# Kernel optimization log

Measured on AMD Instinct MI355X. Metric: run time of the kernel, lower is better.

The kernel has to match this reference:

```python
import jax, jax.numpy as jnp
import numpy as np


def _lstm(x, k, r, b, return_sequences=True):
    # Keras LSTM: gate order i, f, c(g), o; sigmoid recurrent activation, tanh activation.
    # x: [B,T,D], k: [D,4H], r: [H,4H], b: [4H]
    B = x.shape[0]
    H = r.shape[0]
    xk = jnp.einsum('btd,dh->bth', x, k) + b  # precompute input projections for all steps

    def step(carry, xk_t):
        h, c = carry
        z = xk_t + h @ r
        i, f, g, o = jnp.split(z, 4, axis=-1)
        i = jax.nn.sigmoid(i)
        f = jax.nn.sigmoid(f)
        g = jnp.tanh(g)
        o = jax.nn.sigmoid(o)
        c = f * c + i * g
        h = o * jnp.tanh(c)
        return (h, c), h

    h0 = jnp.zeros((B, H), x.dtype)
    (hT, _), hs = jax.lax.scan(step, (h0, jnp.zeros_like(h0)), jnp.swapaxes(xk, 0, 1))
    if return_sequences:
        return jnp.swapaxes(hs, 0, 1)  # [B,T,H]
    return hT  # [B,H]


def _bias(h):
    # Keras unit_forget_bias=True: forget-gate bias initialized to 1
    return jnp.zeros((4 * h,), jnp.float32).at[h:2 * h].set(1.0)


def setup_inputs() -> dict:
    key = jax.random.key(0)
    ks = jax.random.split(key, 20)
    B, T, D = 128, 512, 64
    s = 0.05

    def n(k, shape):
        return jax.random.normal(k, shape, jnp.float32) * s

    inp = {"x": jax.random.normal(ks[0], (B, T, D), jnp.float32)}
    lstm_dims = [(D, 640), (640, 400), (400, 256), (256, 256)]
    i = 1
    for li, (din, h) in enumerate(lstm_dims, 1):
        inp[f"k{li}"] = n(ks[i], (din, 4 * h))
        inp[f"r{li}"] = n(ks[i + 1], (h, 4 * h))
        inp[f"b{li}"] = _bias(h)
        i += 2
    dense_dims = [(256, 512), (512, 256), (256, 128), (128, 64), (64, 16), (16, 3)]
    for li, (din, dout) in enumerate(dense_dims, 1):
        inp[f"wd{li}"] = n(ks[i], (din, dout))
        inp[f"bd{li}"] = jnp.zeros((dout,), jnp.float32)
        i += 1
    return inp


def reference(x, k1, r1, b1, k2, r2, b2, k3, r3, b3, k4, r4, b4,
              wd1, bd1, wd2, bd2, wd3, bd3, wd4, bd4, wd5, bd5, wd6, bd6):
    h = _lstm(x, k1, r1, b1, return_sequences=True)
    h = _lstm(h, k2, r2, b2, return_sequences=True)
    h = _lstm(h, k3, r3, b3, return_sequences=True)
    h = _lstm(h, k4, r4, b4, return_sequences=False)  # [B, 256]
    # Dropout layers are identity at inference (Keras call without training=True)
    h = jax.nn.relu(h @ wd1 + bd1)
    h = jax.nn.relu(h @ wd2 + bd2)
    h = jax.nn.relu(h @ wd3 + bd3)
    h = jax.nn.relu(h @ wd4 + bd4)
    h = jax.nn.relu(h @ wd5 + bd5)
    logits = h @ wd6 + bd6
    return jax.nn.softmax(logits, axis=-1)  # class_count=3 branch
```

## Files before the change

kernel.cpp:

```cpp
#include <hip/hip_runtime.h>
#include <hip/hip_cooperative_groups.h>
#include <cstdint>
#include <cstddef>

namespace cg = cooperative_groups;

typedef _Float16 f16;
typedef _Float16 h8v  __attribute__((ext_vector_type(8)));
typedef float    f32x4 __attribute__((ext_vector_type(4)));

static constexpr int BATCH  = 128;
static constexpr int TSTEPS = 512;
static constexpr int NT     = 256;

static constexpr int TB1 = 80, TB2 = 100, TB3 = 32, TB4 = 32;
static constexpr int TNB   = TB1 + TB2 + TB3 + TB4;
static constexpr int NGRID = TNB + 4;

template<int RING> struct WS {
  static constexpr size_t XT  = 0;
  static constexpr size_t H1  = XT + 512ull * 128 * 64 * 2;
  static constexpr size_t H2  = H1 + (size_t)RING * 128 * 640 * 2 + 64;
  static constexpr size_t H3  = H2 + (size_t)RING * 128 * 400 * 2 + 64;
  static constexpr size_t H4  = H3 + (size_t)RING * 128 * 256 * 2 + 64;
  static constexpr size_t PK1 = H4 + (size_t)RING * 128 * 256 * 2 + 64;
  static constexpr size_t PK2 = PK1 + (size_t)TB1 * 32 * 704  * 2;
  static constexpr size_t PK3 = PK2 + (size_t)TB2 * 16 * 1056 * 2;
  static constexpr size_t PK4 = PK3 + (size_t)TB3 * 32 * 672  * 2;
  static constexpr size_t BAR = PK4 + (size_t)TB4 * 32 * 512  * 2;
  static constexpr size_t ZERO= BAR + 8192;
  static constexpr size_t END = ZERO + 163840;
};

struct KParams {
  const float *x;
  const float *k1, *r1, *b1, *k2, *r2, *b2, *k3, *r3, *b3, *k4, *r4, *b4;
  const float *wd1, *bd1, *wd2, *bd2, *wd3, *bd3, *wd4, *bd4, *wd5, *bd5, *wd6, *bd6;
  float *out;
  char *ws;
};

__device__ __forceinline__ float sigm(float v) { return 1.f / (1.f + expf(-v)); }

__device__ __forceinline__ uint64_t c_load8(const void* p) {
  return __hip_atomic_load((const uint64_t*)p, __ATOMIC_RELAXED, __HIP_MEMORY_SCOPE_AGENT);
}
__device__ __forceinline__ void c_store8(void* p, uint64_t v) {
  __hip_atomic_store((uint64_t*)p, v, __ATOMIC_RELAXED, __HIP_MEMORY_SCOPE_AGENT);
}
__device__ __forceinline__ unsigned short c_load2(const void* p) {
  return __hip_atomic_load((const unsigned short*)p, __ATOMIC_RELAXED, __HIP_MEMORY_SCOPE_AGENT);
}
__device__ __forceinline__ unsigned u_load(const unsigned* p) {
  return __hip_atomic_load(p, __ATOMIC_RELAXED, __HIP_MEMORY_SCOPE_AGENT);
}
__device__ __forceinline__ void u_store(unsigned* p, unsigned v) {
  __hip_atomic_store(p, v, __ATOMIC_RELAXED, __HIP_MEMORY_SCOPE_AGENT);
}
__device__ __forceinline__ void acq_fence() {
  __builtin_amdgcn_fence(__ATOMIC_ACQUIRE, "agent");
}

template<int NBLK>
__device__ void control_role(unsigned* U, int first, int lidx) {
  const int w = threadIdx.x >> 6, lane = threadIdx.x & 63;
  int cand = 1;
  while (cand <= TSTEPS) {
    unsigned v0 = (lane < NBLK)      ? u_load(&U[4 * (first + lane) + w])      : 0xFFFFFFFFu;
    unsigned v1 = (lane + 64 < NBLK) ? u_load(&U[4 * (first + lane + 64) + w]) : 0xFFFFFFFFu;
    unsigned v = v0 < v1 ? v0 : v1;
    if (__all((int)(v >= (unsigned)cand))) {
      if (lane < 16) u_store(&U[1024 + lane * 64 + lidx * 4 + w], (unsigned)cand);
      ++cand;
    }
  }
}

__device__ void prepack_layer(const float* __restrict__ gk, const float* __restrict__ gr,
                              f16* __restrict__ pack, int DIN, int H, int NJ, int KPAD,
                              int TB, int gtid, int gstr) {
  const int KREAL = DIN + H;
  const int NGC = 4 * NJ;
  const long total = (long)TB * NGC * KPAD;
  for (long e = gtid; e < total; e += gstr) {
    const int  k   = (int)(e % KPAD);
    const long r   = e / KPAD;
    const int  n   = (int)(r % NGC);
    const int  blk = (int)(r / NGC);
    const int  g   = n / NJ, jj = n % NJ;
    const int  j   = blk * NJ + jj;
    float v = 0.f;
    if (k < DIN)        v = gk[(size_t)k * 4 * H + (size_t)g * H + j];
    else if (k < KREAL) v = gr[(size_t)(k - DIN) * 4 * H + (size_t)g * H + j];
    pack[e] = (f16)v;
  }
}

#define FETCH(PP, CC) do { \
  _Pragma("unroll") \
  for (int ii_ = 0; ii_ < C; ++ii_) { \
    const int ks_ = (CC) * C + ii_; \
    if (ks_ < KS) { \
      const int k_ = ks_ * 32 + kg; \
      _Pragma("unroll") \
      for (int m_ = 0; m_ < 2; ++m_) { \
        const int bmv_ = m_ ? bm1 : bm0; \
        uint4 v_ = make_uint4(0u, 0u, 0u, 0u); \
        if constexpr (SEQM) { \
          if (k_ < DIN)        v_ = *(const uint4*)(inP + (size_t)bmv_ * DIN + k_); \
          else if (k_ < KREAL) v_ = *(const uint4*)(inH + (size_t)bmv_ * H + (k_ - DIN)); \
        } else { \
          if (k_ < DIN) { \
            const f16* p_ = inP + (size_t)bmv_ * DIN + k_; \
            if constexpr (SEQIN) { \
              ((uint64_t*)&v_)[0] = *(const uint64_t*)p_; \
              ((uint64_t*)&v_)[1] = *(const uint64_t*)(p_ + 4); \
            } else { \
              ((uint64_t*)&v_)[0] = c_load8(p_); \
              ((uint64_t*)&v_)[1] = c_load8(p_ + 4); \
            } \
          } else if (k_ < KREAL) { \
            const f16* p_ = inH + (size_t)bmv_ * H + (k_ - DIN); \
            ((uint64_t*)&v_)[0] = c_load8(p_); \
            ((uint64_t*)&v_)[1] = c_load8(p_ + 4); \
          } \
        } \
        ab[PP][ii_][m_] = v_; \
      } \
    } \
  } \
} while (0)

#define COMPUTE(PP, CC) do { \
  _Pragma("unroll") \
  for (int ii_ = 0; ii_ < C; ++ii_) { \
    const int ks_ = (CC) * C + ii_; \
    if (ks_ < KS) { \
      const int kb_ = ks_ * 32; \
      h8v bf_[NTI]; \
      _Pragma("unroll") \
      for (int nt_ = 0; nt_ < NTI; ++nt_) \
        bf_[nt_] = *(const h8v*)(wlds + (size_t)(nt_ * 16 + l15) * WROW + kb_ + kg); \
      _Pragma("unroll") \
      for (int m_ = 0; m_ < 2; ++m_) { \
        union { uint4 u; h8v v; } af_; \
        af_.u = ab[PP][ii_][m_]; \
        _Pragma("unroll") \
        for (int nt_ = 0; nt_ < NTI; ++nt_) \
          acc[m_][nt_] = __builtin_amdgcn_mfma_f32_16x16x32_f16(af_.v, bf_[nt_], acc[m_][nt_], 0, 0, 0); \
      } \
    } \
  } \
} while (0)

#define WAITOWN do { \
  bool c_ = (lane != 0) || (rcO >= t); \
  while (!__all((int)c_)) { \
    if (!c_) { rcO = (int)u_load(&relp[LIDX * 4 + w]); c_ = (rcO >= t); } \
  } \
} while (0)

template<int DIN, int H, int NJ, int LIDX, bool SEQIN, int RING>
__device__ void lstm_role(int blk, int bid, const f16* lo_base, f16* ownH,
                          const f16* pack, const float* __restrict__ gbias,
                          const f16* zreg, char* smem, unsigned* U) {
  constexpr bool SEQM = (RING == TSTEPS);
  constexpr int KREAL = DIN + H;
  constexpr int KS    = (KREAL + 31) / 32;
  constexpr int KPAD  = KS * 32;
  constexpr int NGC   = 4 * NJ;
  constexpr int NTI   = NGC / 16;
  constexpr int WROW  = KPAD + 8;
  constexpr int ZROW  = 132;
  constexpr int C     = 6;
  constexpr int NC    = (KS + C - 1) / C;
  constexpr int KSX   = DIN / 32;
  constexpr int CH    = KSX / C;
  static_assert(NC <= 6, "NC");
  static_assert(CH <= NC - 1, "CH");
  static_assert(NGC % 16 == 0 && (DIN % 8) == 0 && (KREAL % 8) == 0, "geom");

  const int tid  = threadIdx.x;
  const int w    = tid >> 6, lane = tid & 63;
  const int l15  = lane & 15;
  const int kg   = (lane >> 4) * 8;
  const int bm0  = w * 32 + l15;
  const int bm1  = bm0 + 16;

  f16*   wlds = (f16*)smem;
  float* z    = (float*)(smem + (size_t)NGC * WROW * 2);

  {
    const f16* src = pack + (size_t)blk * NGC * KPAD;
    constexpr int RU = KPAD / 8;
    for (int u = tid; u < NGC * RU; u += NT) {
      const int n = u / RU, k8 = u % RU;
      *(uint4*)(wlds + (size_t)n * WROW + k8 * 8) =
          *(const uint4*)(src + (size_t)n * KPAD + k8 * 8);
    }
  }
  __syncthreads();

  constexpr int JW = NJ / 4;
  const int be  = 32 * w + lane / JW;
  const int jg  = lane % JW;
  const bool epi = (lane < 32 * JW);
  const int j0  = blk * NJ + jg * 4;
  f32x4 bias4[4] = {};
  if (epi) {
    #pragma unroll
    for (int g = 0; g < 4; ++g) bias4[g] = *(const f32x4*)(gbias + (size_t)g * H + j0);
  }
  float cst[4] = {0.f, 0.f, 0.f, 0.f};

  const unsigned* relp = &U[1024 + (bid & 15) * 64];
  int rcI = 0, rcO = 0, rcD = 0;
  (void)rcI; (void)rcD;

  for (int t = 0; t < TSTEPS; ++t) {
    {
      bool c = true;
      if constexpr (LIDX > 0) { if (lane == 0) c = (rcI >= t + 1); }
      if constexpr (CH == 0)  { if (lane == 1) c = (rcO >= t); }
      if constexpr (!SEQM && LIDX < 3) { if (lane == 2) c = (rcD >= t - (RING - 1)); }
      while (!__all((int)c)) {
        if (!c) {
          if constexpr (LIDX > 0) {
            if (lane == 0) { rcI = (int)u_load(&relp[(LIDX - 1) * 4 + w]); c = (rcI >= t + 1); }
          }
          if constexpr (CH == 0) {
            if (lane == 1) { rcO = (int)u_load(&relp[LIDX * 4 + w]); c = (rcO >= t); }
          }
          if constexpr (!SEQM && LIDX < 3) {
            if (lane == 2) { rcD = (int)u_load(&relp[(LIDX + 1) * 4 + w]); c = (rcD >= t - (RING - 1)); }
          }
        }
      }
    }

    const f16* inP = SEQIN ? lo_base + (size_t)t * DIN * BATCH
                           : lo_base + (size_t)(t & (RING - 1)) * DIN * BATCH;
    const f16* inH = (t == 0) ? zreg
                              : ownH + (size_t)((t - 1) & (RING - 1)) * H * BATCH;

    f32x4 acc[2][NTI];
    {
      const f32x4 zz = {0.f, 0.f, 0.f, 0.f};
      #pragma unroll
      for (int m_ = 0; m_ < 2; ++m_)
        #pragma unroll
        for (int nt_ = 0; nt_ < NTI; ++nt_) acc[m_][nt_] = zz;
    }

    uint4 ab[3][C][2];

    FETCH(0, 0);
    if constexpr (NC > 1) { if constexpr (CH == 1) WAITOWN; FETCH(1, 1); }
    if constexpr (NC > 2) { if constexpr (CH == 2) WAITOWN; FETCH(2, 2); }
    COMPUTE(0, 0);
    if constexpr (NC > 1) { if constexpr (NC > 3) { if constexpr (CH == 3) WAITOWN; FETCH(0, 3); } COMPUTE(1, 1); }
    if constexpr (NC > 2) { if constexpr (NC > 4) { if constexpr (CH == 4) WAITOWN; FETCH(1, 4); } COMPUTE(2, 2); }
    if constexpr (NC > 3) { if constexpr (NC > 5) { if constexpr (CH == 5) WAITOWN; FETCH(2, 5); } COMPUTE(0, 3); }
    if constexpr (NC > 4) COMPUTE(1, 4);
    if constexpr (NC > 5) COMPUTE(2, 5);

    #pragma unroll
    for (int m_ = 0; m_ < 2; ++m_)
      #pragma unroll
      for (int nt_ = 0; nt_ < NTI; ++nt_)
        *(f32x4*)(z + (size_t)(nt_ * 16 + l15) * ZROW + w * 32 + m_ * 16 + (lane >> 4) * 4) =
            acc[m_][nt_];

    if (epi) {
      float vi[4], vf[4], vg[4], vo[4];
      #pragma unroll
      for (int q = 0; q < 4; ++q) {
        const int nn = jg * 4 + q;
        vi[q] = z[(size_t)(0 * NJ + nn) * ZROW + be];
        vf[q] = z[(size_t)(1 * NJ + nn) * ZROW + be];
        vg[q] = z[(size_t)(2 * NJ + nn) * ZROW + be];
        vo[q] = z[(size_t)(3 * NJ + nn) * ZROW + be];
      }
      union { f16 h[4]; uint64_t u; } o;
      #pragma unroll
      for (int q = 0; q < 4; ++q) {
        const float ig = sigm(vi[q] + bias4[0][q]);
        const float fg = sigm(vf[q] + bias4[1][q]);
        const float gg = tanhf(vg[q] + bias4[2][q]);
        const float og = sigm(vo[q] + bias4[3][q]);
        cst[q] = fg * cst[q] + ig * gg;
        o.h[q] = (f16)(og * tanhf(cst[q]));
      }
      c_store8(ownH + (size_t)(t & (RING - 1)) * H * BATCH + (size_t)be * H + j0, o.u);
    }
    asm volatile("s_waitcnt vmcnt(0)" ::: "memory");
    if (lane == 0) u_store(&U[4 * bid + w], (unsigned)(t + 1));
  }
}
#undef FETCH
#undef COMPUTE
#undef WAITOWN

__device__ void dense_stage(const float* in, float* outb,
                            const float* __restrict__ w, const float* __restrict__ bias,
                            int din, int dout, bool relu) {
  for (int jc = threadIdx.x; jc < dout; jc += NT) {
    float s = bias[jc];
    for (int d = 0; d < din; ++d) s += in[d] * w[(size_t)d * dout + jc];
    outb[jc] = relu ? fmaxf(s, 0.f) : s;
  }
  __syncthreads();
}

constexpr size_t cmax(size_t a, size_t b) { return a > b ? a : b; }
constexpr size_t wlz(int NGC, int KPAD) {
  return (size_t)NGC * (KPAD + 8) * 2 + (size_t)NGC * 132 * 4;
}
static constexpr size_t SMEM_BYTES =
    cmax(cmax(wlz(32, 704), wlz(16, 1056)),
         cmax(cmax(wlz(32, 672), wlz(32, 512)), (size_t)4096));
static_assert(SMEM_BYTES <= 65536, "LDS");

template<int RING>
__global__ __launch_bounds__(NT, 1) void fused_kernel(KParams p) {
  using L = WS<RING>;
  cg::grid_group grid = cg::this_grid();
  __shared__ __attribute__((aligned(16))) char smem[SMEM_BYTES];

  char* ws = p.ws;
  unsigned* U = (unsigned*)(ws + L::BAR);
  const f16* zreg = (const f16*)(ws + L::ZERO);
  const int tid  = threadIdx.x;
  const int bid  = blockIdx.x;
  const int gtid = bid * NT + tid;
  const int gstr = NGRID * NT;

  prepack_layer(p.k1, p.r1, (f16*)(ws + L::PK1), 64,  640, 8, 704,  TB1, gtid, gstr);
  prepack_layer(p.k2, p.r2, (f16*)(ws + L::PK2), 640, 400, 4, 1056, TB2, gtid, gstr);
  prepack_layer(p.k3, p.r3, (f16*)(ws + L::PK3), 400, 256, 8, 672,  TB3, gtid, gstr);
  prepack_layer(p.k4, p.r4, (f16*)(ws + L::PK4), 256, 256, 8, 512,  TB4, gtid, gstr);

  {
    f16* xT = (f16*)(ws + L::XT);
    const long total = (long)TSTEPS * BATCH * 8;
    for (long u = gtid; u < total; u += gstr) {
      const int  d8 = (int)(u & 7);
      const long r  = u >> 3;
      const int  b  = (int)(r & (BATCH - 1));
      const int  t  = (int)(r >> 7);
      const float* src = p.x + ((size_t)b * TSTEPS + t) * 64 + d8 * 8;
      const float4 v0 = *(const float4*)src;
      const float4 v1 = *(const float4*)(src + 4);
      h8v o;
      o[0] = (f16)v0.x; o[1] = (f16)v0.y; o[2] = (f16)v0.z; o[3] = (f16)v0.w;
      o[4] = (f16)v1.x; o[5] = (f16)v1.y; o[6] = (f16)v1.z; o[7] = (f16)v1.w;
      *(h8v*)(xT + ((size_t)t * BATCH + b) * 64 + d8 * 8) = o;
    }
  }

  grid.sync();
  acq_fence();

  constexpr int TRB2 = TB1, TRB3 = TB1 + TB2, TRB4 = TB1 + TB2 + TB3;
  if (bid >= TNB) {
    const int l = bid - TNB;
    if (l == 0)      control_role<TB1>(U, 0,    0);
    else if (l == 1) control_role<TB2>(U, TRB2, 1);
    else if (l == 2) control_role<TB3>(U, TRB3, 2);
    else             control_role<TB4>(U, TRB4, 3);
  } else if (bid < TRB2) {
    lstm_role< 64, 640, 8, 0, true , RING>(bid, bid, (const f16*)(ws + L::XT),
        (f16*)(ws + L::H1), (const f16*)(ws + L::PK1), p.b1, zreg, smem, U);
  } else if (bid < TRB3) {
    lstm_role<640, 400, 4, 1, false, RING>(bid - TRB2, bid, (const f16*)(ws + L::H1),
        (f16*)(ws + L::H2), (const f16*)(ws + L::PK2), p.b2, zreg, smem, U);
  } else if (bid < TRB4) {
    lstm_role<400, 256, 8, 2, false, RING>(bid - TRB3, bid, (const f16*)(ws + L::H2),
        (f16*)(ws + L::H3), (const f16*)(ws + L::PK3), p.b3, zreg, smem, U);
  } else {
    lstm_role<256, 256, 8, 3, false, RING>(bid - TRB4, bid, (const f16*)(ws + L::H3),
        (f16*)(ws + L::H4), (const f16*)(ws + L::PK4), p.b4, zreg, smem, U);
  }

  if (bid < BATCH) {
    if (tid < 64) {
      bool c = (tid >= 4);
      int rc = 0;
      while (!__all((int)c)) {
        if (!c) {
          rc = (int)u_load(&U[1024 + (bid & 15) * 64 + 3 * 4 + tid]);
          c = (rc >= TSTEPS);
        }
      }
    }
    __syncthreads();
    const int b = bid;
    float* A = (float*)smem;
    float* B = (float*)smem + 512;
    const f16* h4 = (const f16*)(ws + L::H4)
                  + (size_t)((TSTEPS - 1) & (RING - 1)) * 256 * BATCH + (size_t)b * 256;
    for (int d = tid; d < 256; d += NT) {
      union { unsigned short u; f16 h; } cc;
      cc.u = c_load2(h4 + d);
      A[d] = (float)cc.h;
    }
    __syncthreads();
    dense_stage(A, B, p.wd1, p.bd1, 256, 512, true);
    dense_stage(B, A, p.wd2, p.bd2, 512, 256, true);
    dense_stage(A, B, p.wd3, p.bd3, 256, 128, true);
    dense_stage(B, A, p.wd4, p.bd4, 128, 64,  true);
    dense_stage(A, B, p.wd5, p.bd5, 64,  16,  true);
    dense_stage(B, A, p.wd6, p.bd6, 16,  3,   false);
    if (tid == 0) {
      float z0 = A[0], z1 = A[1], z2 = A[2];
      float m  = fmaxf(fmaxf(z0, z1), z2);
      float e0 = expf(z0 - m), e1 = expf(z1 - m), e2 = expf(z2 - m);
      float s  = e0 + e1 + e2;
      p.out[b * 3 + 0] = e0 / s;
      p.out[b * 3 + 1] = e1 / s;
      p.out[b * 3 + 2] = e2 / s;
    }
  }
}

extern "C" void kernel_launch(void* const* d_in, const int* in_sizes, int n_in,
                              void* d_out, int out_size, void* d_ws, size_t ws_size,
                              hipStream_t stream) {
  (void)in_sizes; (void)n_in; (void)out_size;
  KParams prm;
  prm.x  = (const float*)d_in[0];
  prm.k1 = (const float*)d_in[1];  prm.r1 = (const float*)d_in[2];  prm.b1 = (const float*)d_in[3];
  prm.k2 = (const float*)d_in[4];  prm.r2 = (const float*)d_in[5];  prm.b2 = (const float*)d_in[6];
  prm.k3 = (const float*)d_in[7];  prm.r3 = (const float*)d_in[8];  prm.b3 = (const float*)d_in[9];
  prm.k4 = (const float*)d_in[10]; prm.r4 = (const float*)d_in[11]; prm.b4 = (const float*)d_in[12];
  prm.wd1 = (const float*)d_in[13]; prm.bd1 = (const float*)d_in[14];
  prm.wd2 = (const float*)d_in[15]; prm.bd2 = (const float*)d_in[16];
  prm.wd3 = (const float*)d_in[17]; prm.bd3 = (const float*)d_in[18];
  prm.wd4 = (const float*)d_in[19]; prm.bd4 = (const float*)d_in[20];
  prm.wd5 = (const float*)d_in[21]; prm.bd5 = (const float*)d_in[22];
  prm.wd6 = (const float*)d_in[23]; prm.bd6 = (const float*)d_in[24];
  prm.out = (float*)d_out;
  prm.ws  = (char*)d_ws;

  const bool big = ws_size >= WS<TSTEPS>::END;
  const size_t bar_off = big ? WS<TSTEPS>::BAR : WS<4>::BAR;
  hipMemsetAsync((char*)d_ws + bar_off, 0, 8192 + 163840, stream);

  void* args[] = { &prm };
  if (big) {
    hipLaunchCooperativeKernel((void*)fused_kernel<TSTEPS>, dim3(NGRID), dim3(NT),
                               args, 0, stream);
  } else {
    hipLaunchCooperativeKernel((void*)fused_kernel<4>, dim3(NGRID), dim3(NT),
                               args, 0, stream);
  }
}
```

Measured before the change: 4.854 ms.

## Replace control-block progress aggregation with direct per-lane polling of peer flags

Removes the four dedicated control blocks that reduced per-block step counters and republished them. Each LSTM wave now reads the progress flags of all blocks in the producer, same and consumer layers directly, one or two flags per lane, and takes the minimum. This drops an extra hop of latency from every per-step dependency and frees four grid slots. In exchange, many more lanes issue atomic loads to shared counters while spinning, which adds memory and cache contention.

```diff
diff --git a/kernel.cpp b/kernel.cpp
--- a/kernel.cpp
+++ b/kernel.cpp
@@ -15,7 +15,7 @@
 
 static constexpr int TB1 = 80, TB2 = 100, TB3 = 32, TB4 = 32;
 static constexpr int TNB   = TB1 + TB2 + TB3 + TB4;
-static constexpr int NGRID = TNB + 4;
+static constexpr int NGRID = TNB;
 
 template<int RING> struct WS {
   static constexpr size_t XT  = 0;
@@ -60,21 +60,7 @@
 __device__ __forceinline__ void acq_fence() {
   __builtin_amdgcn_fence(__ATOMIC_ACQUIRE, "agent");
 }
-
-template<int NBLK>
-__device__ void control_role(unsigned* U, int first, int lidx) {
-  const int w = threadIdx.x >> 6, lane = threadIdx.x & 63;
-  int cand = 1;
-  while (cand <= TSTEPS) {
-    unsigned v0 = (lane < NBLK)      ? u_load(&U[4 * (first + lane) + w])      : 0xFFFFFFFFu;
-    unsigned v1 = (lane + 64 < NBLK) ? u_load(&U[4 * (first + lane + 64) + w]) : 0xFFFFFFFFu;
-    unsigned v = v0 < v1 ? v0 : v1;
-    if (__all((int)(v >= (unsigned)cand))) {
-      if (lane < 16) u_store(&U[1024 + lane * 64 + lidx * 4 + w], (unsigned)cand);
-      ++cand;
-    }
-  }
-}
+__device__ __forceinline__ int imin2(int a, int b) { return a < b ? a : b; }
 
 __device__ void prepack_layer(const float* __restrict__ gk, const float* __restrict__ gr,
                               f16* __restrict__ pack, int DIN, int H, int NJ, int KPAD,
@@ -154,16 +140,21 @@
 } while (0)
 
 #define WAITOWN do { \
-  bool c_ = (lane != 0) || (rcO >= t); \
+  bool c_ = (oA == nullptr) || (rcO >= t); \
   while (!__all((int)c_)) { \
-    if (!c_) { rcO = (int)u_load(&relp[LIDX * 4 + w]); c_ = (rcO >= t); } \
+    if (!c_) { \
+      int a_ = (int)u_load(oA); \
+      int b_ = oB ? (int)u_load(oB) : 0x7fffffff; \
+      rcO = imin2(a_, b_); c_ = (rcO >= t); \
+    } \
   } \
 } while (0)
 
 template<int DIN, int H, int NJ, int LIDX, bool SEQIN, int RING>
 __device__ void lstm_role(int blk, int bid, const f16* lo_base, f16* ownH,
                           const f16* pack, const float* __restrict__ gbias,
-                          const f16* zreg, char* smem, unsigned* U) {
+                          const f16* zreg, char* smem, unsigned* U,
+                          int pf, int pc, int of, int oc, int nf, int nc) {
   constexpr bool SEQM = (RING == TSTEPS);
   constexpr int KREAL = DIN + H;
   constexpr int KS    = (KREAL + 31) / 32;
@@ -213,27 +204,49 @@
   }
   float cst[4] = {0.f, 0.f, 0.f, 0.f};
 
-  const unsigned* relp = &U[1024 + (bid & 15) * 64];
-  int rcI = 0, rcO = 0, rcD = 0;
-  (void)rcI; (void)rcD;
+  const unsigned* pA = (lane < pc)      ? &U[4 * (pf + lane) + w]      : nullptr;
+  const unsigned* pB = (lane + 64 < pc) ? &U[4 * (pf + lane + 64) + w] : nullptr;
+  const unsigned* oA = (lane < oc)      ? &U[4 * (of + lane) + w]      : nullptr;
+  const unsigned* oB = (lane + 64 < oc) ? &U[4 * (of + lane + 64) + w] : nullptr;
+  const int ncc = SEQM ? 0 : nc;
+  const unsigned* nA = (lane < ncc)      ? &U[4 * (nf + lane) + w]      : nullptr;
+  const unsigned* nB = (lane + 64 < ncc) ? &U[4 * (nf + lane + 64) + w] : nullptr;
+  int rcP = 0, rcO = 0, rcN = 0;
+  (void)rcN;
 
   for (int t = 0; t < TSTEPS; ++t) {
     {
       bool c = true;
-      if constexpr (LIDX > 0) { if (lane == 0) c = (rcI >= t + 1); }
-      if constexpr (CH == 0)  { if (lane == 1) c = (rcO >= t); }
-      if constexpr (!SEQM && LIDX < 3) { if (lane == 2) c = (rcD >= t - (RING - 1)); }
+      if constexpr (LIDX > 0) { if (pA) c = (rcP >= t + 1); }
+      if constexpr (CH == 0)  { if (oA) c = c && (rcO >= t); }
+      if constexpr (!SEQM && LIDX < 3) { if (nA) c = c && (rcN >= t - (RING - 1)); }
       while (!__all((int)c)) {
         if (!c) {
           if constexpr (LIDX > 0) {
-            if (lane == 0) { rcI = (int)u_load(&relp[(LIDX - 1) * 4 + w]); c = (rcI >= t + 1); }
+            if (pA && rcP < t + 1) {
+              int a = (int)u_load(pA);
+              int b = pB ? (int)u_load(pB) : 0x7fffffff;
+              rcP = imin2(a, b);
+            }
           }
           if constexpr (CH == 0) {
-            if (lane == 1) { rcO = (int)u_load(&relp[LIDX * 4 + w]); c = (rcO >= t); }
+            if (oA && rcO < t) {
+              int a = (int)u_load(oA);
+              int b = oB ? (int)u_load(oB) : 0x7fffffff;
+              rcO = imin2(a, b);
+            }
           }
           if constexpr (!SEQM && LIDX < 3) {
-            if (lane == 2) { rcD = (int)u_load(&relp[(LIDX + 1) * 4 + w]); c = (rcD >= t - (RING - 1)); }
+            if (nA && rcN < t - (RING - 1)) {
+              int a = (int)u_load(nA);
+              int b = nB ? (int)u_load(nB) : 0x7fffffff;
+              rcN = imin2(a, b);
+            }
           }
+          c = true;
+          if constexpr (LIDX > 0) { if (pA) c = (rcP >= t + 1); }
+          if constexpr (CH == 0)  { if (oA) c = c && (rcO >= t); }
+          if constexpr (!SEQM && LIDX < 3) { if (nA) c = c && (rcN >= t - (RING - 1)); }
         }
       }
     }
@@ -361,39 +374,33 @@
   grid.sync();
   acq_fence();
 
-  constexpr int TRB2 = TB1, TRB3 = TB1 + TB2, TRB4 = TB1 + TB2 + TB3;
-  if (bid >= TNB) {
-    const int l = bid - TNB;
-    if (l == 0)      control_role<TB1>(U, 0,    0);
-    else if (l == 1) control_role<TB2>(U, TRB2, 1);
-    else if (l == 2) control_role<TB3>(U, TRB3, 2);
-    else             control_role<TB4>(U, TRB4, 3);
-  } else if (bid < TRB2) {
+  constexpr int O2 = TB1, O3 = TB1 + TB2, O4 = TB1 + TB2 + TB3;
+  if (bid < O2) {
     lstm_role< 64, 640, 8, 0, true , RING>(bid, bid, (const f16*)(ws + L::XT),
-        (f16*)(ws + L::H1), (const f16*)(ws + L::PK1), p.b1, zreg, smem, U);
-  } else if (bid < TRB3) {
-    lstm_role<640, 400, 4, 1, false, RING>(bid - TRB2, bid, (const f16*)(ws + L::H1),
-        (f16*)(ws + L::H2), (const f16*)(ws + L::PK2), p.b2, zreg, smem, U);
-  } else if (bid < TRB4) {
-    lstm_role<400, 256, 8, 2, false, RING>(bid - TRB3, bid, (const f16*)(ws + L::H2),
-        (f16*)(ws + L::H3), (const f16*)(ws + L::PK3), p.b3, zreg, smem, U);
+        (f16*)(ws + L::H1), (const f16*)(ws + L::PK1), p.b1, zreg, smem, U,
+        0, 0, 0, TB1, O2, TB2);
+  } else if (bid < O3) {
+    lstm_role<640, 400, 4, 1, false, RING>(bid - O2, bid, (const f16*)(ws + L::H1),
+        (f16*)(ws + L::H2), (const f16*)(ws + L::PK2), p.b2, zreg, smem, U,
+        0, TB1, O2, TB2, O3, TB3);
+  } else if (bid < O4) {
+    lstm_role<400, 256, 8, 2, false, RING>(bid - O3, bid, (const f16*)(ws + L::H2),
+        (f16*)(ws + L::H3), (const f16*)(ws + L::PK3), p.b3, zreg, smem, U,
+        O2, TB2, O3, TB3, O4, TB4);
   } else {
-    lstm_role<256, 256, 8, 3, false, RING>(bid - TRB4, bid, (const f16*)(ws + L::H3),
-        (f16*)(ws + L::H4), (const f16*)(ws + L::PK4), p.b4, zreg, smem, U);
+    lstm_role<256, 256, 8, 3, false, RING>(bid - O4, bid, (const f16*)(ws + L::H3),
+        (f16*)(ws + L::H4), (const f16*)(ws + L::PK4), p.b4, zreg, smem, U,
+        O3, TB3, O4, TB4, 0, 0);
   }
 
   if (bid < BATCH) {
-    if (tid < 64) {
-      bool c = (tid >= 4);
-      int rc = 0;
-      while (!__all((int)c)) {
-        if (!c) {
-          rc = (int)u_load(&U[1024 + (bid & 15) * 64 + 3 * 4 + tid]);
-          c = (rc >= TSTEPS);
-        }
+    {
+      int cond = 1;
+      if (tid < 4 * TB4) cond = ((int)u_load(&U[4 * (O4 + (tid >> 2)) + (tid & 3)]) >= TSTEPS);
+      while (!__syncthreads_and(cond)) {
+        if (!cond) cond = ((int)u_load(&U[4 * (O4 + (tid >> 2)) + (tid & 3)]) >= TSTEPS);
       }
     }
-    __syncthreads();
     const int b = bid;
     float* A = (float*)smem;
     float* B = (float*)smem + 512;
```

New measurement: 6.869 ms. 1.42x slower.
